# Kernel optimization log

Measured on AMD Instinct MI355X. Metric: run time of the kernel, lower is better.

Reference implementation:

```python
import jax, jax.numpy as jnp
import numpy as np

N_NODES = 100000


def sage_conv(x, src, dst, Wl, bl, Wr):
    # mean aggregation of source features at target nodes
    msg_sum = jax.ops.segment_sum(x[src], dst, num_segments=N_NODES)  # [N, C]
    deg = jax.ops.segment_sum(jnp.ones_like(src, dtype=x.dtype), dst, num_segments=N_NODES)
    agg = msg_sum / jnp.maximum(deg, 1.0)[:, None]
    return agg @ Wl + bl + x @ Wr


def setup_inputs() -> dict:
    key = jax.random.key(0)
    ks = jax.random.split(key, 6)
    N, E, C_in, C_hid, C_out = N_NODES, 400000, 128, 256, 64
    x = jax.random.normal(ks[0], (N, C_in), dtype=jnp.float32)
    edge_index = jax.random.randint(ks[1], (2, E), 0, N, dtype=jnp.int64)
    s = 1.0 / np.sqrt(C_in)
    W1l = jax.random.normal(ks[2], (C_in, C_hid), dtype=jnp.float32) * s
    W1r = jax.random.normal(ks[3], (C_in, C_hid), dtype=jnp.float32) * s
    b1 = jnp.zeros((C_hid,), dtype=jnp.float32)
    s2 = 1.0 / np.sqrt(C_hid)
    W2l = jax.random.normal(ks[4], (C_hid, C_out), dtype=jnp.float32) * s2
    W2r = jax.random.normal(ks[5], (C_hid, C_out), dtype=jnp.float32) * s2
    b2 = jnp.zeros((C_out,), dtype=jnp.float32)
    return {"x": x, "edge_index": edge_index, "W1l": W1l, "b1": b1, "W1r": W1r,
            "W2l": W2l, "b2": b2, "W2r": W2r}


def reference(x, edge_index, W1l, b1, W1r, W2l, b2, W2r):
    src, dst = edge_index[0], edge_index[1]
    h = sage_conv(x, src, dst, W1l, b1, W1r)
    h = jax.nn.relu(h)  # dropout is identity in eval mode
    out = sage_conv(h, src, dst, W2l, b2, W2r)
    return out
```

## Files before the change

kernel.cpp:

```cpp
#include <hip/hip_runtime.h>
#include <cstddef>

#define N_NODES 100000
#define E_EDGES 400000
#define C_IN    128
#define C_HID   256
#define C_OUT   64

typedef __attribute__((ext_vector_type(8))) short bf16x8;
typedef __attribute__((ext_vector_type(4))) float f32x4;

__device__ __forceinline__ unsigned short f2bf(float f) {
    union { float f; unsigned u; } x; x.f = f;
    unsigned r = x.u + 0x7fffu + ((x.u >> 16) & 1u);
    return (unsigned short)(r >> 16);
}
__device__ __forceinline__ float bflo(int u) {
    union { int i; float f; } x; x.i = u << 16; return x.f;
}
__device__ __forceinline__ float bfhi(int u) {
    union { int i; float f; } x; x.i = u & 0xffff0000; return x.f;
}

__global__ void hist_kernel(const int* __restrict__ dst, int* __restrict__ deg, int E) {
    int e = blockIdx.x * blockDim.x + threadIdx.x;
    if (e < E) atomicAdd(&deg[dst[e]], 1);
}

__global__ __launch_bounds__(256) void scan_partial(const int* __restrict__ deg,
                                                    int* __restrict__ bsums, int n) {
    __shared__ int red[256];
    int base = blockIdx.x * 2048 + threadIdx.x * 8;
    int s = 0;
    #pragma unroll
    for (int i = 0; i < 8; ++i) { int idx = base + i; if (idx < n) s += deg[idx]; }
    red[threadIdx.x] = s; __syncthreads();
    for (int off = 128; off > 0; off >>= 1) {
        if (threadIdx.x < off) red[threadIdx.x] += red[threadIdx.x + off];
        __syncthreads();
    }
    if (threadIdx.x == 0) bsums[blockIdx.x] = red[0];
}

__global__ __launch_bounds__(64) void scan_bsums(int* __restrict__ bsums, int nb) {
    __shared__ int s[64];
    int t = threadIdx.x;
    s[t] = (t < nb) ? bsums[t] : 0; __syncthreads();
    for (int off = 1; off < 64; off <<= 1) {
        int v = (t >= off) ? s[t - off] : 0;
        __syncthreads();
        s[t] += v;
        __syncthreads();
    }
    if (t < nb) bsums[t] = (t == 0) ? 0 : s[t - 1];
}

__global__ __launch_bounds__(256) void scan_apply(const int* __restrict__ deg,
                                                  const int* __restrict__ bsums,
                                                  int* __restrict__ row_start,
                                                  int* __restrict__ cursor, int n, int E) {
    __shared__ int red[256];
    int t = threadIdx.x;
    int base = blockIdx.x * 2048 + t * 8;
    int v[8]; int s = 0;
    #pragma unroll
    for (int i = 0; i < 8; ++i) { int idx = base + i; v[i] = (idx < n) ? deg[idx] : 0; s += v[i]; }
    red[t] = s; __syncthreads();
    for (int off = 1; off < 256; off <<= 1) {
        int u = (t >= off) ? red[t - off] : 0;
        __syncthreads();
        red[t] += u;
        __syncthreads();
    }
    int run = bsums[blockIdx.x] + ((t == 0) ? 0 : red[t - 1]);
    #pragma unroll
    for (int i = 0; i < 8; ++i) {
        int idx = base + i;
        if (idx < n) { row_start[idx] = run; cursor[idx] = run; run += v[i]; }
    }
    if (blockIdx.x == 0 && t == 0) row_start[n] = E;
}

__global__ void fill_kernel(const int* __restrict__ src, const int* __restrict__ dst,
                            int* __restrict__ cursor, int* __restrict__ nbr, int E) {
    int e = blockIdx.x * blockDim.x + threadIdx.x;
    if (e < E) {
        int pos = atomicAdd(&cursor[dst[e]], 1);
        nbr[pos] = src[e];
    }
}

__global__ void cvt_x_kernel(const float* __restrict__ in,
                             unsigned short* __restrict__ out, int n8) {
    int i = blockIdx.x * blockDim.x + threadIdx.x;
    if (i >= n8) return;
    const float4* p = reinterpret_cast<const float4*>(in) + (size_t)i * 2;
    const float4 a = p[0], b = p[1];
    int4 w;
    w.x = (int)f2bf(a.x) | ((int)f2bf(a.y) << 16);
    w.y = (int)f2bf(a.z) | ((int)f2bf(a.w) << 16);
    w.z = (int)f2bf(b.x) | ((int)f2bf(b.y) << 16);
    w.w = (int)f2bf(b.z) | ((int)f2bf(b.w) << 16);
    reinterpret_cast<int4*>(out)[i] = w;
}

__global__ void gather_mean_bf16(const int* __restrict__ row_start,
                                 const int* __restrict__ nbr,
                                 const unsigned short* __restrict__ xbf,
                                 unsigned short* __restrict__ aggbf, int N) {
    const int gid  = blockIdx.x * blockDim.x + threadIdx.x;
    const int node = gid >> 4;
    const int lane = gid & 15;
    if (node >= N) return;
    const int s = row_start[node];
    const int e = row_start[node + 1];
    float acc[8] = {0.f, 0.f, 0.f, 0.f, 0.f, 0.f, 0.f, 0.f};
    const int4* f = reinterpret_cast<const int4*>(xbf);
    for (int j = s; j < e; ++j) {
        const int4 v = f[(size_t)nbr[j] * 16 + lane];
        acc[0] += bflo(v.x); acc[1] += bfhi(v.x);
        acc[2] += bflo(v.y); acc[3] += bfhi(v.y);
        acc[4] += bflo(v.z); acc[5] += bfhi(v.z);
        acc[6] += bflo(v.w); acc[7] += bfhi(v.w);
    }
    const float inv = 1.0f / (float)((e - s) > 1 ? (e - s) : 1);
    int4 w;
    w.x = (int)f2bf(acc[0] * inv) | ((int)f2bf(acc[1] * inv) << 16);
    w.y = (int)f2bf(acc[2] * inv) | ((int)f2bf(acc[3] * inv) << 16);
    w.z = (int)f2bf(acc[4] * inv) | ((int)f2bf(acc[5] * inv) << 16);
    w.w = (int)f2bf(acc[6] * inv) | ((int)f2bf(acc[7] * inv) << 16);
    reinterpret_cast<int4*>(aggbf)[(size_t)node * 16 + lane] = w;
}

__global__ void gather_out_kernel(const int* __restrict__ row_start,
                                  const int* __restrict__ nbr,
                                  const unsigned short* __restrict__ t2bf,
                                  const float* __restrict__ u,
                                  const float* __restrict__ b2,
                                  float* __restrict__ out, int N) {
    const int gid  = blockIdx.x * blockDim.x + threadIdx.x;
    const int node = gid >> 3;
    const int lane = gid & 7;
    if (node >= N) return;
    const int s = row_start[node];
    const int e = row_start[node + 1];
    float acc[8] = {0.f, 0.f, 0.f, 0.f, 0.f, 0.f, 0.f, 0.f};
    const int4* f = reinterpret_cast<const int4*>(t2bf);
    for (int j = s; j < e; ++j) {
        const int4 v = f[(size_t)nbr[j] * 8 + lane];
        acc[0] += bflo(v.x); acc[1] += bfhi(v.x);
        acc[2] += bflo(v.y); acc[3] += bfhi(v.y);
        acc[4] += bflo(v.z); acc[5] += bfhi(v.z);
        acc[6] += bflo(v.w); acc[7] += bfhi(v.w);
    }
    const float inv = 1.0f / (float)((e - s) > 1 ? (e - s) : 1);
    const float4* up = reinterpret_cast<const float4*>(u) + (size_t)node * 16 + lane * 2;
    const float4 u0 = up[0], u1 = up[1];
    const float4 b0 = reinterpret_cast<const float4*>(b2)[lane * 2];
    const float4 b1 = reinterpret_cast<const float4*>(b2)[lane * 2 + 1];
    float4 o0, o1;
    o0.x = acc[0] * inv + u0.x + b0.x;
    o0.y = acc[1] * inv + u0.y + b0.y;
    o0.z = acc[2] * inv + u0.z + b0.z;
    o0.w = acc[3] * inv + u0.w + b0.w;
    o1.x = acc[4] * inv + u1.x + b1.x;
    o1.y = acc[5] * inv + u1.y + b1.y;
    o1.z = acc[6] * inv + u1.z + b1.z;
    o1.w = acc[7] * inv + u1.w + b1.w;
    float4* op = reinterpret_cast<float4*>(out) + (size_t)node * 16 + lane * 2;
    op[0] = o0; op[1] = o1;
}

__global__ void w1T_kernel(const float* __restrict__ W1l, const float* __restrict__ W1r,
                           unsigned short* __restrict__ W1T) {
    int n = blockIdx.x, k = threadIdx.x;
    float v = (k < 128) ? W1l[(size_t)k * 256 + n] : W1r[(size_t)(k - 128) * 256 + n];
    W1T[(size_t)n * 256 + k] = f2bf(v);
}
__global__ void w2T_kernel(const float* __restrict__ W2l, const float* __restrict__ W2r,
                           unsigned short* __restrict__ WT2) {
    int n = blockIdx.x, k = threadIdx.x;
    float v = (n < 64) ? W2l[(size_t)k * 64 + n] : W2r[(size_t)k * 64 + (n - 64)];
    WT2[(size_t)n * 256 + k] = f2bf(v);
}

__device__ __forceinline__ int swz(int row, int slotByte) {
    return row * 64 + (slotByte ^ (((row >> 1) & 3) << 4));
}

__global__ __launch_bounds__(256) void gemm1_mfma(
        const unsigned short* __restrict__ AggBf,
        const unsigned short* __restrict__ XBf,
        const unsigned short* __restrict__ W1T,
        const float* __restrict__ bias,
        unsigned short* __restrict__ H,
        int M)
{
    __shared__ __align__(16) unsigned short As[64 * 32];
    __shared__ __align__(16) unsigned short Bs[256 * 32];

    const int tid  = threadIdx.x;
    const int wave = tid >> 6, lane = tid & 63;
    const int m0 = blockIdx.x * 64;

    const int a_row = tid >> 2;
    const int a_seg = tid & 3;
    int gm = m0 + a_row; if (gm >= M) gm = M - 1;

    f32x4 acc[4][4];
    #pragma unroll
    for (int m = 0; m < 4; ++m)
        #pragma unroll
        for (int n = 0; n < 4; ++n) acc[m][n] = (f32x4){0.f, 0.f, 0.f, 0.f};

    const int kb = lane >> 4;
    const int lr = lane & 15;

    for (int k0 = 0; k0 < 256; k0 += 32) {
        {
            const unsigned short* srcp = (k0 < 128)
                ? (AggBf + (size_t)gm * 128 + k0 + a_seg * 8)
                : (XBf   + (size_t)gm * 128 + (k0 - 128) + a_seg * 8);
            int4 v = *reinterpret_cast<const int4*>(srcp);
            *reinterpret_cast<int4*>((char*)As + swz(a_row, a_seg * 16)) = v;
        }
        #pragma unroll
        for (int i = 0; i < 4; ++i) {
            int c = tid + 256 * i, row = c >> 2, slot = c & 3;
            int4 v = *reinterpret_cast<const int4*>(W1T + (size_t)row * 256 + k0 + slot * 8);
            *reinterpret_cast<int4*>((char*)Bs + swz(row, slot * 16)) = v;
        }
        __syncthreads();

        bf16x8 af[4], bfr[4];
        #pragma unroll
        for (int m = 0; m < 4; ++m)
            af[m] = *reinterpret_cast<const bf16x8*>((const char*)As + swz(m * 16 + lr, kb * 16));
        #pragma unroll
        for (int n = 0; n < 4; ++n)
            bfr[n] = *reinterpret_cast<const bf16x8*>(
                (const char*)Bs + swz(wave * 64 + n * 16 + lr, kb * 16));
        #pragma unroll
        for (int m = 0; m < 4; ++m)
            #pragma unroll
            for (int n = 0; n < 4; ++n)
                acc[m][n] = __builtin_amdgcn_mfma_f32_16x16x32_bf16(af[m], bfr[n], acc[m][n], 0, 0, 0);
        __syncthreads();
    }

    #pragma unroll
    for (int m = 0; m < 4; ++m) {
        const int gr_base = m0 + m * 16 + (lane >> 4) * 4;
        #pragma unroll
        for (int n = 0; n < 4; ++n) {
            const int gc = wave * 64 + n * 16 + (lane & 15);
            const float b = bias[gc];
            #pragma unroll
            for (int r = 0; r < 4; ++r) {
                const int gr = gr_base + r;
                if (gr < M) {
                    float v = acc[m][n][r] + b;
                    H[(size_t)gr * 256 + gc] = f2bf(fmaxf(v, 0.0f));
                }
            }
        }
    }
}

__global__ __launch_bounds__(256) void gemm2_dual(
        const unsigned short* __restrict__ H,
        const unsigned short* __restrict__ WT2,
        unsigned short* __restrict__ t2bf,
        float* __restrict__ u,
        int M)
{
    __shared__ __align__(16) unsigned short As[64 * 32];
    __shared__ __align__(16) unsigned short Bs[128 * 32];

    const int tid  = threadIdx.x;
    const int wave = tid >> 6, lane = tid & 63;
    const int m0 = blockIdx.x * 64;

    const int a_row = tid >> 2;
    const int a_seg = tid & 3;
    int gm = m0 + a_row; if (gm >= M) gm = M - 1;

    f32x4 acc[4][2];
    #pragma unroll
    for (int m = 0; m < 4; ++m)
        #pragma unroll
        for (int n = 0; n < 2; ++n) acc[m][n] = (f32x4){0.f, 0.f, 0.f, 0.f};

    const int kb = lane >> 4;
    const int lr = lane & 15;

    for (int k0 = 0; k0 < 256; k0 += 32) {
        {
            int4 v = *reinterpret_cast<const int4*>(H + (size_t)gm * 256 + k0 + a_seg * 8);
            *reinterpret_cast<int4*>((char*)As + swz(a_row, a_seg * 16)) = v;
        }
        #pragma unroll
        for (int i = 0; i < 2; ++i) {
            int c = tid + 256 * i, row = c >> 2, slot = c & 3;
            int4 v = *reinterpret_cast<const int4*>(WT2 + (size_t)row * 256 + k0 + slot * 8);
            *reinterpret_cast<int4*>((char*)Bs + swz(row, slot * 16)) = v;
        }
        __syncthreads();

        bf16x8 af[4], bfr[2];
        #pragma unroll
        for (int m = 0; m < 4; ++m)
            af[m] = *reinterpret_cast<const bf16x8*>((const char*)As + swz(m * 16 + lr, kb * 16));
        #pragma unroll
        for (int n = 0; n < 2; ++n)
            bfr[n] = *reinterpret_cast<const bf16x8*>(
                (const char*)Bs + swz(wave * 32 + n * 16 + lr, kb * 16));
        #pragma unroll
        for (int m = 0; m < 4; ++m)
            #pragma unroll
            for (int n = 0; n < 2; ++n)
                acc[m][n] = __builtin_amdgcn_mfma_f32_16x16x32_bf16(af[m], bfr[n], acc[m][n], 0, 0, 0);
        __syncthreads();
    }

    #pragma unroll
    for (int m = 0; m < 4; ++m) {
        const int gr_base = m0 + m * 16 + (lane >> 4) * 4;
        #pragma unroll
        for (int n = 0; n < 2; ++n) {
            const int gc = wave * 32 + n * 16 + (lane & 15);
            #pragma unroll
            for (int r = 0; r < 4; ++r) {
                const int gr = gr_base + r;
                if (gr < M) {
                    if (gc < 64) t2bf[(size_t)gr * 64 + gc] = f2bf(acc[m][n][r]);
                    else         u[(size_t)gr * 64 + (gc - 64)] = acc[m][n][r];
                }
            }
        }
    }
}

extern "C" void kernel_launch(void* const* d_in, const int* in_sizes, int n_in,
                              void* d_out, int out_size, void* d_ws, size_t ws_size,
                              hipStream_t stream) {
    const float* x    = (const float*)d_in[0];
    const int*   eidx = (const int*)d_in[1];
    const float* W1l  = (const float*)d_in[2];
    const float* b1   = (const float*)d_in[3];
    const float* W1r  = (const float*)d_in[4];
    const float* W2l  = (const float*)d_in[5];
    const float* b2   = (const float*)d_in[6];
    const float* W2r  = (const float*)d_in[7];
    float* out = (float*)d_out;

    const int* src = eidx;
    const int* dst = eidx + E_EDGES;
    const int N = N_NODES, E = E_EDGES;
    const int NSCAN = (N + 2047) / 2048;

    int*   deg_i     = (int*)d_ws;
    int*   row_start = deg_i + N;
    int*   cursor    = row_start + (N + 1);
    int*   nbr       = cursor + N;
    int*   bsums     = nbr + E;
    char*  fb        = (char*)(((size_t)(bsums + 64) + 15) & ~(size_t)15);
    unsigned short* W1T    = (unsigned short*)fb;
    unsigned short* WT2    = W1T + 256 * 256;
    unsigned short* x_bf   = WT2 + 128 * 256;
    unsigned short* agg_bf = x_bf + (size_t)N * C_IN;
    unsigned short* h      = agg_bf + (size_t)N * C_IN;
    unsigned short* t2bf   = h + (size_t)N * C_HID;
    float* u = (float*)(((size_t)(t2bf + (size_t)N * C_OUT) + 15) & ~(size_t)15);

    cvt_x_kernel<<<(N * C_IN / 8 + 255) / 256, 256, 0, stream>>>(x, x_bf, N * C_IN / 8);
    w1T_kernel<<<256, 256, 0, stream>>>(W1l, W1r, W1T);
    w2T_kernel<<<128, 256, 0, stream>>>(W2l, W2r, WT2);

    hipMemsetAsync(deg_i, 0, (size_t)N * sizeof(int), stream);
    hist_kernel<<<(E + 255) / 256, 256, 0, stream>>>(dst, deg_i, E);
    scan_partial<<<NSCAN, 256, 0, stream>>>(deg_i, bsums, N);
    scan_bsums<<<1, 64, 0, stream>>>(bsums, NSCAN);
    scan_apply<<<NSCAN, 256, 0, stream>>>(deg_i, bsums, row_start, cursor, N, E);
    fill_kernel<<<(E + 255) / 256, 256, 0, stream>>>(src, dst, cursor, nbr, E);

    gather_mean_bf16<<<((size_t)N * 16 + 255) / 256, 256, 0, stream>>>(
        row_start, nbr, x_bf, agg_bf, N);
    gemm1_mfma<<<(N + 63) / 64, 256, 0, stream>>>(agg_bf, x_bf, W1T, b1, h, N);

    gemm2_dual<<<(N + 63) / 64, 256, 0, stream>>>(h, WT2, t2bf, u, N);
    gather_out_kernel<<<((size_t)N * 8 + 255) / 256, 256, 0, stream>>>(
        row_start, nbr, t2bf, u, b2, out, N);
}
```

Before: 289.9 us.

## Fuse layer-1 and layer-2 GEMMs, keeping hidden activations in shared memory

Merges gemm1 and gemm2 into one kernel. Each block writes its 64x256 bf16 hidden tile into an XOR-swizzled LDS buffer and then runs the second GEMM directly from it. This removes the global write and re-read of the N x 256 hidden tensor and one kernel launch. In exchange, LDS use per block rises by 32 KB, which can lower occupancy, and the second phase still reloads WT2 tiles each k-step.

```diff
diff --git a/kernel.cpp b/kernel.cpp
--- a/kernel.cpp
+++ b/kernel.cpp
@@ -187,17 +187,23 @@
 __device__ __forceinline__ int swz(int row, int slotByte) {
     return row * 64 + (slotByte ^ (((row >> 1) & 3) << 4));
 }
-
-__global__ __launch_bounds__(256) void gemm1_mfma(
+__device__ __forceinline__ int hswz(int row, int byteInRow) {
+    return row * 512 + (byteInRow ^ ((row & 7) << 4));
+}
+
+__global__ __launch_bounds__(256) void gemm12_fused(
         const unsigned short* __restrict__ AggBf,
         const unsigned short* __restrict__ XBf,
         const unsigned short* __restrict__ W1T,
-        const float* __restrict__ bias,
-        unsigned short* __restrict__ H,
+        const float* __restrict__ b1,
+        const unsigned short* __restrict__ WT2,
+        unsigned short* __restrict__ t2bf,
+        float* __restrict__ u,
         int M)
 {
     __shared__ __align__(16) unsigned short As[64 * 32];
     __shared__ __align__(16) unsigned short Bs[256 * 32];
+    __shared__ __align__(16) unsigned short Hs[64 * 256];
 
     const int tid  = threadIdx.x;
     const int wave = tid >> 6, lane = tid & 63;
@@ -207,14 +213,14 @@
     const int a_seg = tid & 3;
     int gm = m0 + a_row; if (gm >= M) gm = M - 1;
 
-    f32x4 acc[4][4];
-    #pragma unroll
-    for (int m = 0; m < 4; ++m)
-        #pragma unroll
-        for (int n = 0; n < 4; ++n) acc[m][n] = (f32x4){0.f, 0.f, 0.f, 0.f};
-
     const int kb = lane >> 4;
     const int lr = lane & 15;
+
+    f32x4 acc[4][4];
+    #pragma unroll
+    for (int m = 0; m < 4; ++m)
+        #pragma unroll
+        for (int n = 0; n < 4; ++n) acc[m][n] = (f32x4){0.f, 0.f, 0.f, 0.f};
 
     for (int k0 = 0; k0 < 256; k0 += 32) {
         {
@@ -250,55 +256,29 @@
 
     #pragma unroll
     for (int m = 0; m < 4; ++m) {
-        const int gr_base = m0 + m * 16 + (lane >> 4) * 4;
+        const int lrow_base = m * 16 + (lane >> 4) * 4;
         #pragma unroll
         for (int n = 0; n < 4; ++n) {
-            const int gc = wave * 64 + n * 16 + (lane & 15);
-            const float b = bias[gc];
+            const int lcol = wave * 64 + n * 16 + (lane & 15);
+            const float b = b1[lcol];
             #pragma unroll
             for (int r = 0; r < 4; ++r) {
-                const int gr = gr_base + r;
-                if (gr < M) {
-                    float v = acc[m][n][r] + b;
-                    H[(size_t)gr * 256 + gc] = f2bf(fmaxf(v, 0.0f));
-                }
+                const int lrow = lrow_base + r;
+                float v = acc[m][n][r] + b;
+                *reinterpret_cast<unsigned short*>((char*)Hs + hswz(lrow, lcol * 2)) =
+                    f2bf(fmaxf(v, 0.0f));
             }
         }
     }
-}
-
-__global__ __launch_bounds__(256) void gemm2_dual(
-        const unsigned short* __restrict__ H,
-        const unsigned short* __restrict__ WT2,
-        unsigned short* __restrict__ t2bf,
-        float* __restrict__ u,
-        int M)
-{
-    __shared__ __align__(16) unsigned short As[64 * 32];
-    __shared__ __align__(16) unsigned short Bs[128 * 32];
-
-    const int tid  = threadIdx.x;
-    const int wave = tid >> 6, lane = tid & 63;
-    const int m0 = blockIdx.x * 64;
-
-    const int a_row = tid >> 2;
-    const int a_seg = tid & 3;
-    int gm = m0 + a_row; if (gm >= M) gm = M - 1;
-
-    f32x4 acc[4][2];
+    __syncthreads();
+
+    f32x4 acc2[4][2];
     #pragma unroll
     for (int m = 0; m < 4; ++m)
         #pragma unroll
-        for (int n = 0; n < 2; ++n) acc[m][n] = (f32x4){0.f, 0.f, 0.f, 0.f};
-
-    const int kb = lane >> 4;
-    const int lr = lane & 15;
+        for (int n = 0; n < 2; ++n) acc2[m][n] = (f32x4){0.f, 0.f, 0.f, 0.f};
 
     for (int k0 = 0; k0 < 256; k0 += 32) {
-        {
-            int4 v = *reinterpret_cast<const int4*>(H + (size_t)gm * 256 + k0 + a_seg * 8);
-            *reinterpret_cast<int4*>((char*)As + swz(a_row, a_seg * 16)) = v;
-        }
         #pragma unroll
         for (int i = 0; i < 2; ++i) {
             int c = tid + 256 * i, row = c >> 2, slot = c & 3;
@@ -309,8 +289,11 @@
 
         bf16x8 af[4], bfr[2];
         #pragma unroll
-        for (int m = 0; m < 4; ++m)
-            af[m] = *reinterpret_cast<const bf16x8*>((const char*)As + swz(m * 16 + lr, kb * 16));
+        for (int m = 0; m < 4; ++m) {
+            const int lrow = m * 16 + lr;
+            af[m] = *reinterpret_cast<const bf16x8*>(
+                (const char*)Hs + hswz(lrow, k0 * 2 + kb * 16));
+        }
         #pragma unroll
         for (int n = 0; n < 2; ++n)
             bfr[n] = *reinterpret_cast<const bf16x8*>(
@@ -319,7 +302,7 @@
         for (int m = 0; m < 4; ++m)
             #pragma unroll
             for (int n = 0; n < 2; ++n)
-                acc[m][n] = __builtin_amdgcn_mfma_f32_16x16x32_bf16(af[m], bfr[n], acc[m][n], 0, 0, 0);
+                acc2[m][n] = __builtin_amdgcn_mfma_f32_16x16x32_bf16(af[m], bfr[n], acc2[m][n], 0, 0, 0);
         __syncthreads();
     }
 
@@ -333,8 +316,8 @@
             for (int r = 0; r < 4; ++r) {
                 const int gr = gr_base + r;
                 if (gr < M) {
-                    if (gc < 64) t2bf[(size_t)gr * 64 + gc] = f2bf(acc[m][n][r]);
-                    else         u[(size_t)gr * 64 + (gc - 64)] = acc[m][n][r];
+                    if (gc < 64) t2bf[(size_t)gr * 64 + gc] = f2bf(acc2[m][n][r]);
+                    else         u[(size_t)gr * 64 + (gc - 64)] = acc2[m][n][r];
                 }
             }
         }
@@ -369,8 +352,7 @@
     unsigned short* WT2    = W1T + 256 * 256;
     unsigned short* x_bf   = WT2 + 128 * 256;
     unsigned short* agg_bf = x_bf + (size_t)N * C_IN;
-    unsigned short* h      = agg_bf + (size_t)N * C_IN;
-    unsigned short* t2bf   = h + (size_t)N * C_HID;
+    unsigned short* t2bf   = agg_bf + (size_t)N * C_IN;
     float* u = (float*)(((size_t)(t2bf + (size_t)N * C_OUT) + 15) & ~(size_t)15);
 
     cvt_x_kernel<<<(N * C_IN / 8 + 255) / 256, 256, 0, stream>>>(x, x_bf, N * C_IN / 8);
@@ -386,9 +368,10 @@
 
     gather_mean_bf16<<<((size_t)N * 16 + 255) / 256, 256, 0, stream>>>(
         row_start, nbr, x_bf, agg_bf, N);
-    gemm1_mfma<<<(N + 63) / 64, 256, 0, stream>>>(agg_bf, x_bf, W1T, b1, h, N);
-
-    gemm2_dual<<<(N + 63) / 64, 256, 0, stream>>>(h, WT2, t2bf, u, N);
+
+    gemm12_fused<<<(N + 63) / 64, 256, 0, stream>>>(
+        agg_bf, x_bf, W1T, b1, WT2, t2bf, u, N);
+
     gather_out_kernel<<<((size_t)N * 8 + 255) / 256, 256, 0, stream>>>(
         row_start, nbr, t2bf, u, b2, out, N);
 }
```

Result: faster. 273.1 us (-5.8%).
